# Optimization experiments

Measured on AMD Instinct MI355X. Metric: run time of the kernel, lower is better.

Reference implementation:

```python
import jax, jax.numpy as jnp
import numpy as np

B, T, D = 2, 2048, 1024
G, E, F = 4, 4, 4096          # num_groups, experts_per_group, d_ff
KG, KE = 2, 1                  # top_k_groups, top_k_experts


def setup_inputs() -> dict:
    key = jax.random.key(0)
    ks = jax.random.split(key, 5)
    init = lambda k, shape, fan: jax.random.normal(k, shape, jnp.float32) / np.sqrt(fan).astype(np.float32)
    x = jax.random.normal(ks[0], (B, T, D), jnp.float32)
    Wg = init(ks[1], (G, D), D)          # group router (torch Linear weight [out,in])
    We = init(ks[2], (G, E, D), D)       # per-group expert routers
    W1 = init(ks[3], (G, E, F, D), D)    # expert up-proj weights
    W2 = init(ks[4], (G, E, D, F), F)    # expert down-proj weights
    return {"x": x, "Wg": Wg, "We": We, "W1": W1, "W2": W2}


def _moe_forward(x, Wg, We, W1, W2):
    b, t, d = x.shape
    xf = x.reshape(b * t, d)                                   # [N, D]
    group_logits = xf @ Wg.T                                   # [N, G]
    gw, gid = jax.lax.top_k(group_logits, KG)                  # [N, KG]
    gw = jax.nn.softmax(gw, axis=-1)
    expert_logits = jnp.einsum('nd,ged->nge', xf, We)          # [N, G, E]
    sel = jnp.take_along_axis(expert_logits, gid[:, :, None], axis=1)  # [N, KG, E]
    ew, eid = jax.lax.top_k(sel, KE)                           # [N, KG, KE]
    ew = jax.nn.softmax(ew, axis=-1)
    w = gw[:, :, None] * ew                                    # [N, KG, KE]
    oh_g = jax.nn.one_hot(gid, G, dtype=xf.dtype)              # [N, KG, G]
    oh_e = jax.nn.one_hot(eid, E, dtype=xf.dtype)              # [N, KG, KE, E]
    # topk group ids are distinct, and expert ids within a group are distinct,
    # so this scatter-by-one-hot exactly reproduces the masked accumulation.
    combine = jnp.einsum('nrg,nrke,nrk->nge', oh_g, oh_e, w)   # [N, G, E]
    out = jnp.zeros_like(xf)
    for g in range(G):
        for e in range(E):
            h = jax.nn.gelu(xf @ W1[g, e].T, approximate=False)  # exact GELU, as nn.GELU()
            out = out + combine[:, g, e, None] * (h @ W2[g, e].T)
    return out.reshape(b, t, d), group_logits.reshape(b, t, G)


def reference(x, Wg, We, W1, W2):
    out, group_logits = _moe_forward(x, Wg, We, W1, W2)
    p = jax.nn.softmax(group_logits, axis=-1)
    lp = jax.nn.log_softmax(group_logits, axis=-1)
    group_entropy = -(p * lp).sum(-1).mean()
    return out, group_logits, group_entropy
```

## Files before the change

### kernel.cpp

```cpp
#include <hip/hip_runtime.h>
#include <hip/hip_bf16.h>

#define NTOK 4096
#define DDIM 1024
#define GG 4
#define EE 4
#define FF 4096
#define NEXP 16
#define OUT_ELEMS 4194304
#define GL_OFF 4194304
#define ENT_OFF 4210688

typedef float f32x4 __attribute__((ext_vector_type(4)));
typedef short short8 __attribute__((ext_vector_type(8)));

__device__ inline unsigned short f2bf(float f) {
  unsigned int u = __float_as_uint(f);
  unsigned int rounding = 0x7FFFu + ((u >> 16) & 1u);
  return (unsigned short)((u + rounding) >> 16);
}
__device__ inline unsigned int pack2(float f0, float f1) {
  return (unsigned int)f2bf(f0) | ((unsigned int)f2bf(f1) << 16);
}

__global__ void cvt_kernel(const float* __restrict__ x, unsigned short* __restrict__ xb) {
  int idx = blockIdx.x * 256 + threadIdx.x;
  const float4* p = reinterpret_cast<const float4*>(x) + (size_t)idx * 2;
  float4 a = p[0], b = p[1];
  uint4 v;
  v.x = pack2(a.x, a.y); v.y = pack2(a.z, a.w);
  v.z = pack2(b.x, b.y); v.w = pack2(b.z, b.w);
  reinterpret_cast<uint4*>(xb)[idx] = v;
}

__global__ __launch_bounds__(256) void routing_kernel(
    const float* __restrict__ x, const float* __restrict__ Wg,
    const float* __restrict__ We, float* __restrict__ out,
    int* __restrict__ cnt, int* __restrict__ tokL, int* __restrict__ hrwL,
    float* __restrict__ wslot) {
  int wave = threadIdx.x >> 6, lane = threadIdx.x & 63;
  int token = blockIdx.x * 4 + wave;
  const float4* xr = reinterpret_cast<const float4*>(x + (size_t)token * DDIM);
  float4 xv[4];
#pragma unroll
  for (int c = 0; c < 4; c++) xv[c] = xr[c * 64 + lane];

  auto dotrow = [&](const float* w) -> float {
    const float4* w4 = reinterpret_cast<const float4*>(w);
    float s = 0.f;
#pragma unroll
    for (int c = 0; c < 4; c++) {
      float4 wv = w4[c * 64 + lane];
      s += xv[c].x * wv.x + xv[c].y * wv.y + xv[c].z * wv.z + xv[c].w * wv.w;
    }
#pragma unroll
    for (int off = 32; off; off >>= 1) s += __shfl_xor(s, off, 64);
    return s;
  };

  float gl[GG];
#pragma unroll
  for (int g = 0; g < GG; g++) gl[g] = dotrow(Wg + g * DDIM);

  int g0 = 0;
  for (int g = 1; g < GG; g++) if (gl[g] > gl[g0]) g0 = g;
  int g1 = -1;
  for (int g = 0; g < GG; g++) { if (g == g0) continue; if (g1 < 0 || gl[g] > gl[g1]) g1 = g; }
  float e1 = __expf(gl[g1] - gl[g0]);
  float inv = 1.f / (1.f + e1);
  float w0 = inv, w1 = e1 * inv;

  int gsel[2] = {g0, g1};
  float wsel[2] = {w0, w1};
  int esel[2];
#pragma unroll
  for (int r = 0; r < 2; r++) {
    float el[EE];
#pragma unroll
    for (int e = 0; e < EE; e++) el[e] = dotrow(We + ((size_t)gsel[r] * EE + e) * DDIM);
    int best = 0;
    for (int e = 1; e < EE; e++) if (el[e] > el[best]) best = e;
    esel[r] = best;
  }

  float m = gl[0];
  for (int g = 1; g < GG; g++) m = fmaxf(m, gl[g]);
  float se = 0.f;
  for (int g = 0; g < GG; g++) se += __expf(gl[g] - m);
  float lse = __logf(se);
  float ent = 0.f;
  for (int g = 0; g < GG; g++) {
    float lp = gl[g] - m - lse;
    ent -= __expf(lp) * lp;
  }

  if (lane == 0) {
    for (int g = 0; g < GG; g++) out[GL_OFF + token * GG + g] = gl[g];
    atomicAdd(out + ENT_OFF, ent * (1.0f / NTOK));
    for (int r = 0; r < 2; r++) {
      int ge = gsel[r] * EE + esel[r];
      int pos = atomicAdd(cnt + ge, 1);
      tokL[ge * NTOK + pos] = token;
      hrwL[ge * NTOK + pos] = r * NTOK + token;
      wslot[r * NTOK + token] = wsel[r];
    }
  }
}

#define LDSP 40

__global__ __launch_bounds__(256) void up_kernel(
    const unsigned short* __restrict__ xb, const float* __restrict__ W1,
    const int* __restrict__ cnt, const int* __restrict__ tokL,
    const int* __restrict__ hrwL, unsigned short* __restrict__ H) {
  int ge = blockIdx.z, mt = blockIdx.y;
  int count = cnt[ge];
  if (mt * 64 >= count) return;
  int f0 = blockIdx.x * 64;

  __shared__ short As[64 * LDSP];
  __shared__ short Bs[64 * LDSP];
  __shared__ int rowsS[64];
  __shared__ int destS[64];

  int t = threadIdx.x;
  if (t < 64) {
    int i = mt * 64 + t;
    bool valid = i < count;
    rowsS[t] = valid ? tokL[ge * NTOK + i] : 0;
    destS[t] = valid ? hrwL[ge * NTOK + i] : -1;
  }
  __syncthreads();

  int srow = t >> 2;
  int schunk = (t & 3) * 8;
  const unsigned short* aptr = xb + (size_t)rowsS[srow] * DDIM + schunk;
  const float* bptr = W1 + ((size_t)ge * FF + (f0 + srow)) * DDIM + schunk;
  short* aw = &As[srow * LDSP + schunk];
  short* bw = &Bs[srow * LDSP + schunk];

  int wv = t >> 6, lane = t & 63;
  int m0 = wv * 16;
  int kg = (lane >> 4) * 8;
  const short8* afp = reinterpret_cast<const short8*>(&As[(m0 + (lane & 15)) * LDSP + kg]);

  f32x4 acc[4] = {};

  for (int kb = 0; kb < DDIM; kb += 32) {
    uint4 av = *reinterpret_cast<const uint4*>(aptr + kb);
    float4 b0 = *reinterpret_cast<const float4*>(bptr + kb);
    float4 b1 = *reinterpret_cast<const float4*>(bptr + kb + 4);
    *reinterpret_cast<uint4*>(aw) = av;
    uint4 bv;
    bv.x = pack2(b0.x, b0.y); bv.y = pack2(b0.z, b0.w);
    bv.z = pack2(b1.x, b1.y); bv.w = pack2(b1.z, b1.w);
    *reinterpret_cast<uint4*>(bw) = bv;
    __syncthreads();
    short8 af = *afp;
#pragma unroll
    for (int j = 0; j < 4; j++) {
      short8 bf = *reinterpret_cast<const short8*>(&Bs[(j * 16 + (lane & 15)) * LDSP + kg]);
      acc[j] = __builtin_amdgcn_mfma_f32_16x16x32_bf16(af, bf, acc[j], 0, 0, 0);
    }
    __syncthreads();
  }

  int rl = (lane >> 4) * 4;
  int col = lane & 15;
#pragma unroll
  for (int j = 0; j < 4; j++) {
    int f = f0 + j * 16 + col;
#pragma unroll
    for (int i2 = 0; i2 < 4; i2++) {
      int hr = destS[m0 + rl + i2];
      if (hr >= 0) {
        float v = acc[j][i2];
        float gel = 0.5f * v * (1.0f + erff(v * 0.70710678118654752f));
        H[(size_t)hr * FF + f] = f2bf(gel);
      }
    }
  }
}

__global__ __launch_bounds__(256) void down_kernel(
    const unsigned short* __restrict__ H, const float* __restrict__ W2,
    const int* __restrict__ cnt, const int* __restrict__ hrwL,
    float* __restrict__ Y) {
  int ge = blockIdx.z, mt = blockIdx.y;
  int count = cnt[ge];
  if (mt * 64 >= count) return;
  int d0 = blockIdx.x * 64;

  __shared__ short As[64 * LDSP];
  __shared__ short Bs[64 * LDSP];
  __shared__ int rowsS[64];

  int t = threadIdx.x;
  if (t < 64) {
    int i = mt * 64 + t;
    bool valid = i < count;
    rowsS[t] = valid ? hrwL[ge * NTOK + i] : -1;
  }
  __syncthreads();

  int srow = t >> 2;
  int schunk = (t & 3) * 8;
  int arow = rowsS[srow] < 0 ? 0 : rowsS[srow];
  const unsigned short* aptr = H + (size_t)arow * FF + schunk;
  const float* bptr = W2 + ((size_t)ge * DDIM + (d0 + srow)) * FF + schunk;
  short* aw = &As[srow * LDSP + schunk];
  short* bw = &Bs[srow * LDSP + schunk];

  int wv = t >> 6, lane = t & 63;
  int m0 = wv * 16;
  int kg = (lane >> 4) * 8;
  const short8* afp = reinterpret_cast<const short8*>(&As[(m0 + (lane & 15)) * LDSP + kg]);

  f32x4 acc[4] = {};

  for (int kb = 0; kb < FF; kb += 32) {
    uint4 av = *reinterpret_cast<const uint4*>(aptr + kb);
    float4 b0 = *reinterpret_cast<const float4*>(bptr + kb);
    float4 b1 = *reinterpret_cast<const float4*>(bptr + kb + 4);
    *reinterpret_cast<uint4*>(aw) = av;
    uint4 bv;
    bv.x = pack2(b0.x, b0.y); bv.y = pack2(b0.z, b0.w);
    bv.z = pack2(b1.x, b1.y); bv.w = pack2(b1.z, b1.w);
    *reinterpret_cast<uint4*>(bw) = bv;
    __syncthreads();
    short8 af = *afp;
#pragma unroll
    for (int j = 0; j < 4; j++) {
      short8 bf = *reinterpret_cast<const short8*>(&Bs[(j * 16 + (lane & 15)) * LDSP + kg]);
      acc[j] = __builtin_amdgcn_mfma_f32_16x16x32_bf16(af, bf, acc[j], 0, 0, 0);
    }
    __syncthreads();
  }

  int rl = (lane >> 4) * 4;
  int col = lane & 15;
#pragma unroll
  for (int j = 0; j < 4; j++) {
    int d = d0 + j * 16 + col;
#pragma unroll
    for (int i2 = 0; i2 < 4; i2++) {
      int hr = rowsS[m0 + rl + i2];
      if (hr >= 0) Y[(size_t)hr * DDIM + d] = acc[j][i2];
    }
  }
}

__global__ void combine_kernel(const float* __restrict__ Y,
                               const float* __restrict__ wslot,
                               float* __restrict__ out) {
  int idx = blockIdx.x * 256 + threadIdx.x;
  int token = idx >> 8;
  float w0 = wslot[token], w1 = wslot[NTOK + token];
  float4 a = reinterpret_cast<const float4*>(Y)[idx];
  float4 b = reinterpret_cast<const float4*>(Y + (size_t)NTOK * DDIM)[idx];
  float4 o;
  o.x = w0 * a.x + w1 * b.x;
  o.y = w0 * a.y + w1 * b.y;
  o.z = w0 * a.z + w1 * b.z;
  o.w = w0 * a.w + w1 * b.w;
  reinterpret_cast<float4*>(out)[idx] = o;
}

extern "C" void kernel_launch(void* const* d_in, const int* in_sizes, int n_in,
                              void* d_out, int out_size, void* d_ws, size_t ws_size,
                              hipStream_t stream) {
  const float* x  = (const float*)d_in[0];
  const float* Wg = (const float*)d_in[1];
  const float* We = (const float*)d_in[2];
  const float* W1 = (const float*)d_in[3];
  const float* W2 = (const float*)d_in[4];
  float* out = (float*)d_out;
  char* ws = (char*)d_ws;

  int* cnt = (int*)(ws);
  int* tokL = (int*)(ws + 1024);
  int* hrwL = (int*)(ws + 1024 + 262144);
  float* wslot = (float*)(ws + 1024 + 524288);
  unsigned short* xb = (unsigned short*)(ws + (1 << 20));
  unsigned short* H  = (unsigned short*)(ws + (1 << 20) + 8388608);
  float* Y = (float*)(ws + (1 << 20) + 8388608 + 67108864);

  hipMemsetAsync(d_out, 0, (size_t)out_size * sizeof(float), stream);
  hipMemsetAsync(ws, 0, 1024, stream);

  cvt_kernel<<<2048, 256, 0, stream>>>(x, xb);
  routing_kernel<<<1024, 256, 0, stream>>>(x, Wg, We, out, cnt, tokL, hrwL, wslot);
  up_kernel<<<dim3(FF / 64, 64, NEXP), 256, 0, stream>>>(xb, W1, cnt, tokL, hrwL, H);
  down_kernel<<<dim3(DDIM / 64, 64, NEXP), 256, 0, stream>>>(H, W2, cnt, hrwL, Y);
  combine_kernel<<<4096, 256, 0, stream>>>(Y, wslot, out);
}
```

Measured before the change: 1.096 ms.

## Use 128x128 tiles with 4x4 MFMA per wave and direct global-to-LDS loads

The expert GEMM kernels move from 64x64 block tiles, where each wave computes 16x64, to 128x128 tiles where each wave computes a 64x64 sub-tile with a 4x4 grid of MFMA accumulators. This raises arithmetic intensity per LDS load and halves how often the fp32 weights are re-read per token tile. Activation rows are loaded straight into LDS with global_load_lds instead of going through registers. Weight conversion to bf16 uses a cheaper rounding (round-half-up instead of round-to-nearest-even), and LDS rows are no longer padded, which risks bank conflicts. Larger tiles also waste more work on partially filled expert tiles and cut the number of blocks.

```diff
diff --git a/kernel.cpp b/kernel.cpp
--- a/kernel.cpp
+++ b/kernel.cpp
@@ -22,6 +22,16 @@
 __device__ inline unsigned int pack2(float f0, float f1) {
   return (unsigned int)f2bf(f0) | ((unsigned int)f2bf(f1) << 16);
 }
+__device__ inline unsigned int pack2rn(float f0, float f1) {
+  unsigned int u0 = __float_as_uint(f0), u1 = __float_as_uint(f1);
+  return ((u0 + 0x8000u) >> 16) | ((u1 + 0x8000u) & 0xFFFF0000u);
+}
+
+__device__ __forceinline__ void gload_lds16(const void* g, void* l) {
+  __builtin_amdgcn_global_load_lds(
+      (const __attribute__((address_space(1))) unsigned int*)g,
+      (__attribute__((address_space(3))) unsigned int*)l, 16, 0, 0);
+}
 
 __global__ void cvt_kernel(const float* __restrict__ x, unsigned short* __restrict__ xb) {
   int idx = blockIdx.x * 256 + threadIdx.x;
@@ -107,76 +117,87 @@
   }
 }
 
-#define LDSP 40
-
 __global__ __launch_bounds__(256) void up_kernel(
     const unsigned short* __restrict__ xb, const float* __restrict__ W1,
     const int* __restrict__ cnt, const int* __restrict__ tokL,
     const int* __restrict__ hrwL, unsigned short* __restrict__ H) {
   int ge = blockIdx.z, mt = blockIdx.y;
   int count = cnt[ge];
-  if (mt * 64 >= count) return;
-  int f0 = blockIdx.x * 64;
-
-  __shared__ short As[64 * LDSP];
-  __shared__ short Bs[64 * LDSP];
-  __shared__ int rowsS[64];
-  __shared__ int destS[64];
+  if (mt * 128 >= count) return;
+  int f0 = blockIdx.x * 128;
+
+  __shared__ unsigned short As[128 * 32];
+  __shared__ unsigned short Bs[128 * 32];
+  __shared__ int rowsS[128];
+  __shared__ int destS[128];
 
   int t = threadIdx.x;
-  if (t < 64) {
-    int i = mt * 64 + t;
+  int w = t >> 6, lane = t & 63;
+  if (t < 128) {
+    int i = mt * 128 + t;
     bool valid = i < count;
     rowsS[t] = valid ? tokL[ge * NTOK + i] : 0;
     destS[t] = valid ? hrwL[ge * NTOK + i] : -1;
   }
   __syncthreads();
 
-  int srow = t >> 2;
-  int schunk = (t & 3) * 8;
-  const unsigned short* aptr = xb + (size_t)rowsS[srow] * DDIM + schunk;
-  const float* bptr = W1 + ((size_t)ge * FF + (f0 + srow)) * DDIM + schunk;
-  short* aw = &As[srow * LDSP + schunk];
-  short* bw = &Bs[srow * LDSP + schunk];
-
-  int wv = t >> 6, lane = t & 63;
-  int m0 = wv * 16;
+  int r0 = w * 16 + (lane >> 2);
+  const unsigned short* a0 = xb + (size_t)rowsS[r0] * DDIM + (lane & 3) * 8;
+  const unsigned short* a1 = xb + (size_t)rowsS[r0 + 64] * DDIM + (lane & 3) * 8;
+  unsigned short* l0 = &As[w * 512];
+  unsigned short* l1 = &As[2048 + w * 512];
+
+  const float* bsrc = W1 + ((size_t)ge * FF + (f0 + (t >> 1))) * DDIM + (t & 1) * 16;
+  unsigned short* bdst = &Bs[(t >> 1) * 32 + (t & 1) * 16];
+
+  int m0 = (w >> 1) * 64, n0w = (w & 1) * 64;
   int kg = (lane >> 4) * 8;
-  const short8* afp = reinterpret_cast<const short8*>(&As[(m0 + (lane & 15)) * LDSP + kg]);
-
-  f32x4 acc[4] = {};
+  int rl = lane & 15;
+
+  f32x4 acc[4][4] = {};
 
   for (int kb = 0; kb < DDIM; kb += 32) {
-    uint4 av = *reinterpret_cast<const uint4*>(aptr + kb);
-    float4 b0 = *reinterpret_cast<const float4*>(bptr + kb);
-    float4 b1 = *reinterpret_cast<const float4*>(bptr + kb + 4);
-    *reinterpret_cast<uint4*>(aw) = av;
-    uint4 bv;
-    bv.x = pack2(b0.x, b0.y); bv.y = pack2(b0.z, b0.w);
-    bv.z = pack2(b1.x, b1.y); bv.w = pack2(b1.z, b1.w);
-    *reinterpret_cast<uint4*>(bw) = bv;
+    gload_lds16(a0 + kb, l0);
+    gload_lds16(a1 + kb, l1);
+    float4 q0 = *reinterpret_cast<const float4*>(bsrc + kb);
+    float4 q1 = *reinterpret_cast<const float4*>(bsrc + kb + 4);
+    float4 q2 = *reinterpret_cast<const float4*>(bsrc + kb + 8);
+    float4 q3 = *reinterpret_cast<const float4*>(bsrc + kb + 12);
+    uint4 v0, v1;
+    v0.x = pack2rn(q0.x, q0.y); v0.y = pack2rn(q0.z, q0.w);
+    v0.z = pack2rn(q1.x, q1.y); v0.w = pack2rn(q1.z, q1.w);
+    v1.x = pack2rn(q2.x, q2.y); v1.y = pack2rn(q2.z, q2.w);
+    v1.z = pack2rn(q3.x, q3.y); v1.w = pack2rn(q3.z, q3.w);
+    *reinterpret_cast<uint4*>(bdst) = v0;
+    *reinterpret_cast<uint4*>(bdst + 8) = v1;
     __syncthreads();
-    short8 af = *afp;
+    short8 af[4];
+#pragma unroll
+    for (int i = 0; i < 4; i++)
+      af[i] = *reinterpret_cast<const short8*>(&As[(m0 + i * 16 + rl) * 32 + kg]);
 #pragma unroll
     for (int j = 0; j < 4; j++) {
-      short8 bf = *reinterpret_cast<const short8*>(&Bs[(j * 16 + (lane & 15)) * LDSP + kg]);
-      acc[j] = __builtin_amdgcn_mfma_f32_16x16x32_bf16(af, bf, acc[j], 0, 0, 0);
+      short8 bf = *reinterpret_cast<const short8*>(&Bs[(n0w + j * 16 + rl) * 32 + kg]);
+#pragma unroll
+      for (int i = 0; i < 4; i++)
+        acc[i][j] = __builtin_amdgcn_mfma_f32_16x16x32_bf16(af[i], bf, acc[i][j], 0, 0, 0);
     }
     __syncthreads();
   }
 
-  int rl = (lane >> 4) * 4;
-  int col = lane & 15;
-#pragma unroll
-  for (int j = 0; j < 4; j++) {
-    int f = f0 + j * 16 + col;
-#pragma unroll
-    for (int i2 = 0; i2 < 4; i2++) {
-      int hr = destS[m0 + rl + i2];
+  int re = (lane >> 4) * 4;
+#pragma unroll
+  for (int i = 0; i < 4; i++) {
+#pragma unroll
+    for (int e = 0; e < 4; e++) {
+      int hr = destS[m0 + i * 16 + re + e];
       if (hr >= 0) {
-        float v = acc[j][i2];
-        float gel = 0.5f * v * (1.0f + erff(v * 0.70710678118654752f));
-        H[(size_t)hr * FF + f] = f2bf(gel);
+#pragma unroll
+        for (int j = 0; j < 4; j++) {
+          float v = acc[i][j][e];
+          float gel = 0.5f * v * (1.0f + erff(v * 0.70710678118654752f));
+          H[(size_t)hr * FF + f0 + n0w + j * 16 + rl] = f2bf(gel);
+        }
       }
     }
   }
@@ -188,64 +209,80 @@
     float* __restrict__ Y) {
   int ge = blockIdx.z, mt = blockIdx.y;
   int count = cnt[ge];
-  if (mt * 64 >= count) return;
-  int d0 = blockIdx.x * 64;
-
-  __shared__ short As[64 * LDSP];
-  __shared__ short Bs[64 * LDSP];
-  __shared__ int rowsS[64];
+  if (mt * 128 >= count) return;
+  int d0 = blockIdx.x * 128;
+
+  __shared__ unsigned short As[128 * 32];
+  __shared__ unsigned short Bs[128 * 32];
+  __shared__ int rowsS[128];
 
   int t = threadIdx.x;
-  if (t < 64) {
-    int i = mt * 64 + t;
+  int w = t >> 6, lane = t & 63;
+  if (t < 128) {
+    int i = mt * 128 + t;
     bool valid = i < count;
     rowsS[t] = valid ? hrwL[ge * NTOK + i] : -1;
   }
   __syncthreads();
 
-  int srow = t >> 2;
-  int schunk = (t & 3) * 8;
-  int arow = rowsS[srow] < 0 ? 0 : rowsS[srow];
-  const unsigned short* aptr = H + (size_t)arow * FF + schunk;
-  const float* bptr = W2 + ((size_t)ge * DDIM + (d0 + srow)) * FF + schunk;
-  short* aw = &As[srow * LDSP + schunk];
-  short* bw = &Bs[srow * LDSP + schunk];
-
-  int wv = t >> 6, lane = t & 63;
-  int m0 = wv * 16;
+  int r0 = w * 16 + (lane >> 2);
+  int ar0 = rowsS[r0] < 0 ? 0 : rowsS[r0];
+  int ar1 = rowsS[r0 + 64] < 0 ? 0 : rowsS[r0 + 64];
+  const unsigned short* a0 = H + (size_t)ar0 * FF + (lane & 3) * 8;
+  const unsigned short* a1 = H + (size_t)ar1 * FF + (lane & 3) * 8;
+  unsigned short* l0 = &As[w * 512];
+  unsigned short* l1 = &As[2048 + w * 512];
+
+  const float* bsrc = W2 + ((size_t)ge * DDIM + (d0 + (t >> 1))) * FF + (t & 1) * 16;
+  unsigned short* bdst = &Bs[(t >> 1) * 32 + (t & 1) * 16];
+
+  int m0 = (w >> 1) * 64, n0w = (w & 1) * 64;
   int kg = (lane >> 4) * 8;
-  const short8* afp = reinterpret_cast<const short8*>(&As[(m0 + (lane & 15)) * LDSP + kg]);
-
-  f32x4 acc[4] = {};
+  int rl = lane & 15;
+
+  f32x4 acc[4][4] = {};
 
   for (int kb = 0; kb < FF; kb += 32) {
-    uint4 av = *reinterpret_cast<const uint4*>(aptr + kb);
-    float4 b0 = *reinterpret_cast<const float4*>(bptr + kb);
-    float4 b1 = *reinterpret_cast<const float4*>(bptr + kb + 4);
-    *reinterpret_cast<uint4*>(aw) = av;
-    uint4 bv;
-    bv.x = pack2(b0.x, b0.y); bv.y = pack2(b0.z, b0.w);
-    bv.z = pack2(b1.x, b1.y); bv.w = pack2(b1.z, b1.w);
-    *reinterpret_cast<uint4*>(bw) = bv;
+    gload_lds16(a0 + kb, l0);
+    gload_lds16(a1 + kb, l1);
+    float4 q0 = *reinterpret_cast<const float4*>(bsrc + kb);
+    float4 q1 = *reinterpret_cast<const float4*>(bsrc + kb + 4);
+    float4 q2 = *reinterpret_cast<const float4*>(bsrc + kb + 8);
+    float4 q3 = *reinterpret_cast<const float4*>(bsrc + kb + 12);
+    uint4 v0, v1;
+    v0.x = pack2rn(q0.x, q0.y); v0.y = pack2rn(q0.z, q0.w);
+    v0.z = pack2rn(q1.x, q1.y); v0.w = pack2rn(q1.z, q1.w);
+    v1.x = pack2rn(q2.x, q2.y); v1.y = pack2rn(q2.z, q2.w);
+    v1.z = pack2rn(q3.x, q3.y); v1.w = pack2rn(q3.z, q3.w);
+    *reinterpret_cast<uint4*>(bdst) = v0;
+    *reinterpret_cast<uint4*>(bdst + 8) = v1;
     __syncthreads();
-    short8 af = *afp;
+    short8 af[4];
+#pragma unroll
+    for (int i = 0; i < 4; i++)
+      af[i] = *reinterpret_cast<const short8*>(&As[(m0 + i * 16 + rl) * 32 + kg]);
 #pragma unroll
     for (int j = 0; j < 4; j++) {
-      short8 bf = *reinterpret_cast<const short8*>(&Bs[(j * 16 + (lane & 15)) * LDSP + kg]);
-      acc[j] = __builtin_amdgcn_mfma_f32_16x16x32_bf16(af, bf, acc[j], 0, 0, 0);
+      short8 bf = *reinterpret_cast<const short8*>(&Bs[(n0w + j * 16 + rl) * 32 + kg]);
+#pragma unroll
+      for (int i = 0; i < 4; i++)
+        acc[i][j] = __builtin_amdgcn_mfma_f32_16x16x32_bf16(af[i], bf, acc[i][j], 0, 0, 0);
     }
     __syncthreads();
   }
 
-  int rl = (lane >> 4) * 4;
-  int col = lane & 15;
-#pragma unroll
-  for (int j = 0; j < 4; j++) {
-    int d = d0 + j * 16 + col;
-#pragma unroll
-    for (int i2 = 0; i2 < 4; i2++) {
-      int hr = rowsS[m0 + rl + i2];
-      if (hr >= 0) Y[(size_t)hr * DDIM + d] = acc[j][i2];
+  int re = (lane >> 4) * 4;
+#pragma unroll
+  for (int i = 0; i < 4; i++) {
+#pragma unroll
+    for (int e = 0; e < 4; e++) {
+      int hr = rowsS[m0 + i * 16 + re + e];
+      if (hr >= 0) {
+#pragma unroll
+        for (int j = 0; j < 4; j++) {
+          Y[(size_t)hr * DDIM + d0 + n0w + j * 16 + rl] = acc[i][j][e];
+        }
+      }
     }
   }
 }
@@ -290,7 +327,7 @@
 
   cvt_kernel<<<2048, 256, 0, stream>>>(x, xb);
   routing_kernel<<<1024, 256, 0, stream>>>(x, Wg, We, out, cnt, tokL, hrwL, wslot);
-  up_kernel<<<dim3(FF / 64, 64, NEXP), 256, 0, stream>>>(xb, W1, cnt, tokL, hrwL, H);
-  down_kernel<<<dim3(DDIM / 64, 64, NEXP), 256, 0, stream>>>(H, W2, cnt, hrwL, Y);
+  up_kernel<<<dim3(FF / 128, 32, NEXP), 256, 0, stream>>>(xb, W1, cnt, tokL, hrwL, H);
+  down_kernel<<<dim3(DDIM / 128, 32, NEXP), 256, 0, stream>>>(H, W2, cnt, hrwL, Y);
   combine_kernel<<<4096, 256, 0, stream>>>(Y, wslot, out);
 }
```

After: 1.004 ms. 1.09x faster.
